# Performance work log

Hardware: AMD Instinct MI355X
Metric: run time of the kernel (lower is better)

## Reference

```python
import jax, jax.numpy as jnp
import numpy as np

N, E, G = 50000, 250000, 512
I_DIM, H, E_DIM = 32, 32, 16


def setup_inputs() -> dict:
    key = jax.random.key(0)
    ks = jax.random.split(key, 16)
    f32 = jnp.float32

    def w(k, shape, fan_in):
        return (jax.random.normal(k, shape, f32) / np.float32(np.sqrt(fan_in)))

    return {
        "x": jax.random.normal(ks[0], (N, I_DIM), f32),
        "edge_attr": jax.random.normal(ks[1], (E, E_DIM), f32),
        "edge_index": jax.random.randint(ks[2], (2, E), 0, N),
        "batch": jnp.sort(jax.random.randint(ks[3], (N,), 0, G)),
        "alpha": jnp.float32(1.0),
        # lin0
        "W0": w(ks[4], (I_DIM, H), I_DIM), "b0": jnp.zeros((H,), f32),
        # NNConv edge-weight MLP: Linear(e,h) -> ReLU -> Linear(h, h*h)
        "We1": w(ks[5], (E_DIM, H), E_DIM), "be1": jnp.zeros((H,), f32),
        "We2": w(ks[6], (H, H * H), H) * 0.1, "be2": jnp.zeros((H * H,), f32),
        # NNConv root weight + bias
        "Wroot": w(ks[7], (H, H), H), "bconv": jnp.zeros((H,), f32),
        # GRU (torch layout: gates [r,z,n] stacked -> 3H rows)
        "Wih": w(ks[8], (3 * H, H), H), "bih": jnp.zeros((3 * H,), f32),
        "Whh": w(ks[9], (3 * H, H), H), "bhh": jnp.zeros((3 * H,), f32),
        # lin1 head (label)
        "W1a": w(ks[10], (H, H), H), "b1a": jnp.zeros((H,), f32),
        "W1b": w(ks[11], (H, 1), H), "b1b": jnp.zeros((1,), f32),
        # lin2 head (domain)
        "W2a": w(ks[12], (H, H), H), "b2a": jnp.zeros((H,), f32),
        "W2b": w(ks[13], (H, 2), H), "b2b": jnp.zeros((2,), f32),
    }


def _segment_mean(vals, ids, num_segments):
    s = jax.ops.segment_sum(vals, ids, num_segments=num_segments)
    cnt = jax.ops.segment_sum(jnp.ones((vals.shape[0], 1), vals.dtype), ids,
                              num_segments=num_segments)
    return s / jnp.maximum(cnt, 1.0)


def reference(x, edge_attr, edge_index, batch, alpha,
              W0, b0, We1, be1, We2, be2, Wroot, bconv,
              Wih, bih, Whh, bhh, W1a, b1a, W1b, b1b, W2a, b2a, W2b, b2b):
    n_nodes = x.shape[0]
    src, dst = edge_index[0], edge_index[1]

    # lin0
    out = jax.nn.relu(x @ W0 + b0)          # [N, H]
    h = out                                   # GRU hidden (single layer, 1 step)

    # edge MLP -> per-edge [H, H] weights (constant across the 3 iterations)
    ew = jax.nn.relu(edge_attr @ We1 + be1) @ We2 + be2   # [E, H*H]
    ew = ew.reshape(-1, H, H)                              # [E, H, H]

    for _ in range(3):
        # NNConv: gather source states, per-edge matmul, scatter-mean to dst
        msg = jnp.einsum('eh,eho->eo', out[src], ew)       # [E, H]
        agg = _segment_mean(msg, dst, n_nodes)             # [N, H]
        m = jax.nn.relu(agg + out @ Wroot + bconv)         # [N, H]
        # GRU step (torch gate order r, z, n)
        gi = m @ Wih.T + bih
        gh = h @ Whh.T + bhh
        r = jax.nn.sigmoid(gi[:, :H] + gh[:, :H])
        z = jax.nn.sigmoid(gi[:, H:2 * H] + gh[:, H:2 * H])
        n = jnp.tanh(gi[:, 2 * H:] + r * gh[:, 2 * H:])
        h = (1.0 - z) * n + z * h
        out = h

    # gradient reversal is identity in forward
    num_graphs = G
    pooled = _segment_mean(out, batch, num_graphs)          # [G, H]

    label_out = (jax.nn.relu(pooled @ W1a + b1a) @ W1b + b1b).reshape(-1)  # [G]
    domain_out = jax.nn.relu(pooled @ W2a + b2a) @ W2b + b2b               # [G, 2]
    return label_out, jax.nn.log_softmax(domain_out, axis=1)
```

## Files before the change

kernel.cpp:

```cpp
#include <hip/hip_runtime.h>

typedef unsigned short u16;
typedef unsigned int u32;

#define NN 50000
#define EE 250000
#define GG 512

typedef __bf16 bf16x8 __attribute__((ext_vector_type(8)));
typedef float  f32x4  __attribute__((ext_vector_type(4)));

__device__ __forceinline__ u16 f2bfu(float f) {
    __bf16 b = (__bf16)f; u16 u; __builtin_memcpy(&u, &b, 2); return u;
}
__device__ __forceinline__ float sigf(float x) { return 1.f / (1.f + expf(-x)); }

__global__ void prep_B(const float* __restrict__ We2, const float* __restrict__ be2,
                       u16* __restrict__ Bg) {
    int idx = blockIdx.x * blockDim.x + threadIdx.x;
    if (idx >= 33 * 1024) return;
    int kk = idx >> 10, off = idx & 1023;
    int ct = off >> 9, l = (off >> 3) & 63, j = off & 7;
    int q = l >> 4, c = l & 15, o = c + 16 * ct;
    float v;
    if (kk < 32) v = We2[(32 * kk + 8 * q + j) * 32 + o];
    else         v = be2[(8 * q + j) * 32 + o];
    Bg[idx] = f2bfu(v);
}

__global__ void prep_WT(const float* __restrict__ Wih, const float* __restrict__ Whh,
                        float4* __restrict__ wta, float2* __restrict__ wtb) {
    int t = blockIdx.x * blockDim.x + threadIdx.x;
    if (t >= 1024) return;
    int k = t >> 5, j = t & 31;
    wta[t] = make_float4(Wih[j * 32 + k], Wih[(32 + j) * 32 + k],
                         Wih[(64 + j) * 32 + k], Whh[j * 32 + k]);
    wtb[t] = make_float2(Whh[(32 + j) * 32 + k], Whh[(64 + j) * 32 + k]);
}

__global__ void prep_edges(const float* __restrict__ ea, const float* __restrict__ We1,
                           const float* __restrict__ be1, u16* __restrict__ tmat) {
    int e = blockIdx.x * blockDim.x + threadIdx.x;
    if (e >= EE) return;
    const float4* ep = (const float4*)(ea + (size_t)e * 16);
    float a[16];
#pragma unroll
    for (int i = 0; i < 4; i++) {
        float4 v = ep[i];
        a[4 * i] = v.x; a[4 * i + 1] = v.y; a[4 * i + 2] = v.z; a[4 * i + 3] = v.w;
    }
    u32 outw[16];
#pragma unroll
    for (int p = 0; p < 16; p++) {
        float acc0 = be1[2 * p], acc1 = be1[2 * p + 1];
#pragma unroll
        for (int k = 0; k < 16; k++) {
            acc0 += a[k] * We1[k * 32 + 2 * p];
            acc1 += a[k] * We1[k * 32 + 2 * p + 1];
        }
        acc0 = fmaxf(acc0, 0.f); acc1 = fmaxf(acc1, 0.f);
        outw[p] = (u32)f2bfu(acc0) | ((u32)f2bfu(acc1) << 16);
    }
    uint4* op = (uint4*)(tmat + (size_t)e * 32);
#pragma unroll
    for (int i = 0; i < 4; i++)
        op[i] = make_uint4(outw[4 * i], outw[4 * i + 1], outw[4 * i + 2], outw[4 * i + 3]);
}

__global__ void lin0_k(const float* __restrict__ x, const float* __restrict__ W0,
                       const float* __restrict__ b0, float* __restrict__ hf,
                       u16* __restrict__ cur) {
    int n = blockIdx.x * blockDim.x + threadIdx.x;
    if (n >= NN) return;
    const float4* xp = (const float4*)(x + (size_t)n * 32);
    float a[32];
#pragma unroll
    for (int i = 0; i < 8; i++) {
        float4 v = xp[i];
        a[4 * i] = v.x; a[4 * i + 1] = v.y; a[4 * i + 2] = v.z; a[4 * i + 3] = v.w;
    }
    float o[32];
#pragma unroll 4
    for (int c = 0; c < 32; c++) {
        float acc = b0[c];
#pragma unroll
        for (int k = 0; k < 32; k++) acc += a[k] * W0[k * 32 + c];
        o[c] = fmaxf(acc, 0.f);
    }
    float4* hp = (float4*)(hf + (size_t)n * 32);
#pragma unroll
    for (int i = 0; i < 8; i++) hp[i] = make_float4(o[4 * i], o[4 * i + 1], o[4 * i + 2], o[4 * i + 3]);
    uint4* cp = (uint4*)(cur + (size_t)n * 32);
#pragma unroll
    for (int i = 0; i < 4; i++) {
        u32 p0 = (u32)f2bfu(o[8 * i + 0]) | ((u32)f2bfu(o[8 * i + 1]) << 16);
        u32 p1 = (u32)f2bfu(o[8 * i + 2]) | ((u32)f2bfu(o[8 * i + 3]) << 16);
        u32 p2 = (u32)f2bfu(o[8 * i + 4]) | ((u32)f2bfu(o[8 * i + 5]) << 16);
        u32 p3 = (u32)f2bfu(o[8 * i + 6]) | ((u32)f2bfu(o[8 * i + 7]) << 16);
        cp[i] = make_uint4(p0, p1, p2, p3);
    }
}

__global__ void hist_k(const int* __restrict__ ei, const int* __restrict__ batch,
                       int* __restrict__ degc, int* __restrict__ gcnt) {
    int i = blockIdx.x * blockDim.x + threadIdx.x;
    if (i < EE) atomicAdd(degc + ei[EE + i], 1);
    if (i < NN) atomicAdd(gcnt + batch[i], 1);
}

__global__ void degfin_k(const int* __restrict__ degc, float* __restrict__ dinv) {
    int n = blockIdx.x * blockDim.x + threadIdx.x;
    if (n >= NN) return;
    int c = degc[n];
    dinv[n] = 1.f / (float)(c > 0 ? c : 1);
}

__global__ __launch_bounds__(512) void msg_k(const u16* __restrict__ cur,
                                             const u16* __restrict__ tmat,
                                             const int* __restrict__ ei,
                                             const u16* __restrict__ Bg,
                                             float* __restrict__ agg) {
    __shared__ uint4 Bl[4096];
    const uint4* Bgv = (const uint4*)Bg;
    for (int i = threadIdx.x; i < 4096; i += 512) Bl[i] = Bgv[i];
    __syncthreads();
    const u16* Bl16 = (const u16*)Bl;

    int l = threadIdx.x & 63;
    int q = l >> 4, r = l & 15;
    int wid = (blockIdx.x * blockDim.x + threadIdx.x) >> 6;
    int nw  = (gridDim.x * blockDim.x) >> 6;

    for (int tile = wid; tile < EE / 16; tile += nw) {
        int eb = tile * 16;
        int srow = ei[eb + r];
        bf16x8 sv = *reinterpret_cast<const bf16x8*>(cur + (size_t)srow * 32 + q * 8);
        float sf[8];
#pragma unroll
        for (int j = 0; j < 8; j++) sf[j] = (float)sv[j];
        const uint4* tp = reinterpret_cast<const uint4*>(tmat + (size_t)(eb + r) * 32);
        f32x4 acc0 = {0.f, 0.f, 0.f, 0.f}, acc1 = {0.f, 0.f, 0.f, 0.f};
#pragma unroll
        for (int kq = 0; kq < 4; kq++) {
            uint4 tw4 = tp[kq];
            u32 tws[4] = {tw4.x, tw4.y, tw4.z, tw4.w};
#pragma unroll
            for (int du = 0; du < 4; du++) {
                u32 w = tws[du];
#pragma unroll
                for (int hl = 0; hl < 2; hl++) {
                    int kk = kq * 8 + du * 2 + hl;
                    float tf = __uint_as_float(hl ? (w & 0xffff0000u) : (w << 16));
                    bf16x8 av;
#pragma unroll
                    for (int j = 0; j < 8; j++) av[j] = (__bf16)(tf * sf[j]);
                    bf16x8 b0 = *reinterpret_cast<const bf16x8*>(Bl16 + kk * 1024 + l * 8);
                    bf16x8 b1 = *reinterpret_cast<const bf16x8*>(Bl16 + kk * 1024 + 512 + l * 8);
                    acc0 = __builtin_amdgcn_mfma_f32_16x16x32_bf16(av, b0, acc0, 0, 0, 0);
                    acc1 = __builtin_amdgcn_mfma_f32_16x16x32_bf16(av, b1, acc1, 0, 0, 0);
                }
            }
        }
        {
            bf16x8 b0 = *reinterpret_cast<const bf16x8*>(Bg + 32 * 1024 + l * 8);
            bf16x8 b1 = *reinterpret_cast<const bf16x8*>(Bg + 32 * 1024 + 512 + l * 8);
            acc0 = __builtin_amdgcn_mfma_f32_16x16x32_bf16(sv, b0, acc0, 0, 0, 0);
            acc1 = __builtin_amdgcn_mfma_f32_16x16x32_bf16(sv, b1, acc1, 0, 0, 0);
        }
#pragma unroll
        for (int j = 0; j < 4; j++) {
            int d = ei[EE + eb + 4 * q + j];
            atomicAdd(agg + (size_t)d * 32 + r,      acc0[j]);
            atomicAdd(agg + (size_t)d * 32 + 16 + r, acc1[j]);
        }
    }
}

__global__ __launch_bounds__(512) void node_update_v4(
        float* __restrict__ hf, u16* __restrict__ cur,
        const float* __restrict__ agg, const float* __restrict__ dinv,
        const float* __restrict__ Wroot, const float* __restrict__ bconv,
        const float4* __restrict__ wta_g, const float2* __restrict__ wtb_g,
        const float* __restrict__ bih, const float* __restrict__ bhh) {
    __shared__ float  wroot_l[1024];
    __shared__ float4 wta_l[1024];
    __shared__ float2 wtb_l[1024];
    __shared__ float  h_l[32 * 66];
    __shared__ float  m_l[32 * 66];
    __shared__ float  bias_l[192];

    const int t = threadIdx.x;
    const int w = t >> 6;
    const int lane = t & 63;
    const int nb = blockIdx.x * 64;
    const int n = nb + lane;
    const int nc = (n < NN) ? n : (NN - 1);

    if (t < 256) ((float4*)wroot_l)[t] = ((const float4*)Wroot)[t];
    wta_l[t] = wta_g[t]; wta_l[t + 512] = wta_g[t + 512];
    ((float4*)wtb_l)[t] = ((const float4*)wtb_g)[t];
    if (t < 192) bias_l[t] = (t < 96) ? bih[t] : bhh[t - 96];

    {
        const int nl = t >> 3, ch = t & 7;
        const int ng = nb + nl;
        const int ngc = (ng < NN) ? ng : (NN - 1);
        float4 v = *(const float4*)(hf + (size_t)ngc * 32 + ch * 4);
        h_l[(ch * 4 + 0) * 66 + nl] = v.x;
        h_l[(ch * 4 + 1) * 66 + nl] = v.y;
        h_l[(ch * 4 + 2) * 66 + nl] = v.z;
        h_l[(ch * 4 + 3) * 66 + nl] = v.w;
    }
    __syncthreads();

    const int c0 = w * 4;
    {
        const float di = dinv[nc];
        float4 ag = *(const float4*)(agg + (size_t)nc * 32 + c0);
        float a0 = bconv[c0 + 0] + ag.x * di;
        float a1 = bconv[c0 + 1] + ag.y * di;
        float a2 = bconv[c0 + 2] + ag.z * di;
        float a3 = bconv[c0 + 3] + ag.w * di;
#pragma unroll 4
        for (int k = 0; k < 32; k++) {
            float hk = h_l[k * 66 + lane];
            float4 wr = *(const float4*)&wroot_l[k * 32 + c0];
            a0 = fmaf(hk, wr.x, a0); a1 = fmaf(hk, wr.y, a1);
            a2 = fmaf(hk, wr.z, a2); a3 = fmaf(hk, wr.w, a3);
        }
        m_l[(c0 + 0) * 66 + lane] = fmaxf(a0, 0.f);
        m_l[(c0 + 1) * 66 + lane] = fmaxf(a1, 0.f);
        m_l[(c0 + 2) * 66 + lane] = fmaxf(a2, 0.f);
        m_l[(c0 + 3) * 66 + lane] = fmaxf(a3, 0.f);
    }
    __syncthreads();

    float outv[4];
#pragma unroll
    for (int half = 0; half < 2; half++) {
        const int j0 = c0 + half * 2;
        float air0 = 0.f, aiz0 = 0.f, ain0 = 0.f, ahr0 = 0.f, ahz0 = 0.f, ahn0 = 0.f;
        float air1 = 0.f, aiz1 = 0.f, ain1 = 0.f, ahr1 = 0.f, ahz1 = 0.f, ahn1 = 0.f;
#pragma unroll 4
        for (int k = 0; k < 32; k++) {
            float mk = m_l[k * 66 + lane];
            float hk = h_l[k * 66 + lane];
            float4 wa0 = wta_l[k * 32 + j0];
            float2 wb0 = wtb_l[k * 32 + j0];
            float4 wa1 = wta_l[k * 32 + j0 + 1];
            float2 wb1 = wtb_l[k * 32 + j0 + 1];
            air0 = fmaf(mk, wa0.x, air0); aiz0 = fmaf(mk, wa0.y, aiz0);
            ain0 = fmaf(mk, wa0.z, ain0); ahr0 = fmaf(hk, wa0.w, ahr0);
            ahz0 = fmaf(hk, wb0.x, ahz0); ahn0 = fmaf(hk, wb0.y, ahn0);
            air1 = fmaf(mk, wa1.x, air1); aiz1 = fmaf(mk, wa1.y, aiz1);
            ain1 = fmaf(mk, wa1.z, ain1); ahr1 = fmaf(hk, wa1.w, ahr1);
            ahz1 = fmaf(hk, wb1.x, ahz1); ahn1 = fmaf(hk, wb1.y, ahn1);
        }
#pragma unroll
        for (int jj = 0; jj < 2; jj++) {
            const int j = j0 + jj;
            float air = jj ? air1 : air0, aiz = jj ? aiz1 : aiz0, ain = jj ? ain1 : ain0;
            float ahr = jj ? ahr1 : ahr0, ahz = jj ? ahz1 : ahz0, ahn = jj ? ahn1 : ahn0;
            float r = sigf(air + ahr + bias_l[j] + bias_l[96 + j]);
            float z = sigf(aiz + ahz + bias_l[32 + j] + bias_l[128 + j]);
            float g = tanhf(ain + bias_l[64 + j] + r * (ahn + bias_l[160 + j]));
            float ho = h_l[j * 66 + lane];
            outv[half * 2 + jj] = (1.f - z) * g + z * ho;
        }
    }
    __syncthreads();

#pragma unroll
    for (int i = 0; i < 4; i++) m_l[(c0 + i) * 66 + lane] = outv[i];
    __syncthreads();

    {
        const int nl = t >> 3, q = (t & 7) * 4;
        const int ng = nb + nl;
        if (ng < NN) {
            float4 v = make_float4(m_l[(q + 0) * 66 + nl], m_l[(q + 1) * 66 + nl],
                                   m_l[(q + 2) * 66 + nl], m_l[(q + 3) * 66 + nl]);
            *(float4*)(hf + (size_t)ng * 32 + q) = v;
            u32 p0 = (u32)f2bfu(v.x) | ((u32)f2bfu(v.y) << 16);
            u32 p1 = (u32)f2bfu(v.z) | ((u32)f2bfu(v.w) << 16);
            *(uint2*)(cur + (size_t)ng * 32 + q) = make_uint2(p0, p1);
        }
    }
}

__global__ void pool_k(const float* __restrict__ hf, const int* __restrict__ batch,
                       float* __restrict__ gsum) {
    int n = blockIdx.x * blockDim.x + threadIdx.x;
    if (n >= NN) return;
    int g = batch[n];
#pragma unroll 8
    for (int o = 0; o < 32; o++) atomicAdd(gsum + g * 32 + o, hf[(size_t)n * 32 + o]);
}

__global__ void head_k(const float* __restrict__ gsum, const int* __restrict__ gcnt,
                       const float* __restrict__ W1a, const float* __restrict__ b1a,
                       const float* __restrict__ W1b, const float* __restrict__ b1b,
                       const float* __restrict__ W2a, const float* __restrict__ b2a,
                       const float* __restrict__ W2b, const float* __restrict__ b2b,
                       float* __restrict__ dout) {
    int g = blockIdx.x * blockDim.x + threadIdx.x;
    if (g >= GG) return;
    int c0 = gcnt[g];
    float rc = 1.f / (float)(c0 > 0 ? c0 : 1);
    float p[32];
#pragma unroll
    for (int i = 0; i < 32; i++) p[i] = gsum[g * 32 + i] * rc;
    float lab = b1b[0];
#pragma unroll 4
    for (int c = 0; c < 32; c++) {
        float acc = b1a[c];
#pragma unroll
        for (int k = 0; k < 32; k++) acc += p[k] * W1a[k * 32 + c];
        lab += fmaxf(acc, 0.f) * W1b[c];
    }
    float d0 = b2b[0], d1 = b2b[1];
#pragma unroll 4
    for (int c = 0; c < 32; c++) {
        float acc = b2a[c];
#pragma unroll
        for (int k = 0; k < 32; k++) acc += p[k] * W2a[k * 32 + c];
        float t = fmaxf(acc, 0.f);
        d0 += t * W2b[c * 2];
        d1 += t * W2b[c * 2 + 1];
    }
    float mx = fmaxf(d0, d1);
    float ls = mx + logf(expf(d0 - mx) + expf(d1 - mx));
    dout[g] = lab;
    dout[GG + g * 2]     = d0 - ls;
    dout[GG + g * 2 + 1] = d1 - ls;
}

extern "C" void kernel_launch(void* const* d_in, const int* in_sizes, int n_in,
                              void* d_out, int out_size, void* d_ws, size_t ws_size,
                              hipStream_t stream) {
    const float* x   = (const float*)d_in[0];
    const float* ea  = (const float*)d_in[1];
    const int* ei    = (const int*)d_in[2];
    const int* batch = (const int*)d_in[3];
    const float* W0 = (const float*)d_in[5],  *b0 = (const float*)d_in[6];
    const float* We1 = (const float*)d_in[7], *be1 = (const float*)d_in[8];
    const float* We2 = (const float*)d_in[9], *be2 = (const float*)d_in[10];
    const float* Wroot = (const float*)d_in[11], *bconv = (const float*)d_in[12];
    const float* Wih = (const float*)d_in[13], *bih = (const float*)d_in[14];
    const float* Whh = (const float*)d_in[15], *bhh = (const float*)d_in[16];
    const float* W1a = (const float*)d_in[17], *b1a = (const float*)d_in[18];
    const float* W1b = (const float*)d_in[19], *b1b = (const float*)d_in[20];
    const float* W2a = (const float*)d_in[21], *b2a = (const float*)d_in[22];
    const float* W2b = (const float*)d_in[23], *b2b = (const float*)d_in[24];
    float* dout = (float*)d_out;

    char* w = (char*)d_ws;
    u16*   tmat = (u16*)w;    w += (size_t)EE * 32 * 2;
    u16*   Bg   = (u16*)w;    w += 33 * 1024 * 2 + 512;
    float* hf   = (float*)w;  w += (size_t)NN * 32 * 4;
    u16*   cur  = (u16*)w;    w += (size_t)NN * 32 * 2;
    float* agg  = (float*)w;  w += (size_t)NN * 32 * 4;
    float* dinv = (float*)w;  w += 200192;
    int*   degc = (int*)w;    w += 200192;
    float* gsum = (float*)w;  w += (size_t)GG * 32 * 4;
    int*   gcnt = (int*)w;    w += 2048;
    float4* wta_g = (float4*)w; w += 1024 * 16;
    float2* wtb_g = (float2*)w; w += 1024 * 8;

    hipMemsetAsync(degc, 0, NN * 4, stream);
    hipMemsetAsync(gcnt, 0, GG * 4, stream);
    hipMemsetAsync(gsum, 0, GG * 32 * 4, stream);

    prep_B<<<132, 256, 0, stream>>>(We2, be2, Bg);
    prep_WT<<<4, 256, 0, stream>>>(Wih, Whh, wta_g, wtb_g);
    prep_edges<<<(EE + 255) / 256, 256, 0, stream>>>(ea, We1, be1, tmat);
    lin0_k<<<(NN + 255) / 256, 256, 0, stream>>>(x, W0, b0, hf, cur);
    hist_k<<<(EE + 255) / 256, 256, 0, stream>>>(ei, batch, degc, gcnt);
    degfin_k<<<(NN + 255) / 256, 256, 0, stream>>>(degc, dinv);

    for (int it = 0; it < 3; it++) {
        hipMemsetAsync(agg, 0, (size_t)NN * 32 * 4, stream);
        msg_k<<<512, 512, 0, stream>>>(cur, tmat, ei, Bg, agg);
        node_update_v4<<<(NN + 63) / 64, 512, 0, stream>>>(hf, cur, agg, dinv,
                                                           Wroot, bconv, wta_g, wtb_g, bih, bhh);
    }

    pool_k<<<(NN + 255) / 256, 256, 0, stream>>>(hf, batch, gsum);
    head_k<<<2, 256, 0, stream>>>(gsum, gcnt, W1a, b1a, W1b, b1b, W2a, b2a, W2b, b2b, dout);
}
```

Before: 713.6 us.

## Sort edges by destination via counting sort; coalesce atomics in msg and pooling

Adds a counting sort of edges by destination (histogram, two-level scan, scatter) and writes the per-edge hidden features and source/destination arrays in that sorted order. The message kernel then reads sorted src/dst and merges consecutive equal-destination contributions in registers before issuing atomics, which cuts atomic traffic and improves locality of the agg writes. Pooling is rewritten so each wavefront walks contiguous nodes and flushes only when the graph id changes, instead of doing one atomic per node per feature. Extra preprocessing kernels and a scatter with atomics add one-off cost, and summation order now differs.

```diff
diff --git a/kernel.cpp b/kernel.cpp
--- a/kernel.cpp
+++ b/kernel.cpp
@@ -38,8 +38,72 @@
     wtb[t] = make_float2(Whh[(32 + j) * 32 + k], Whh[(64 + j) * 32 + k]);
 }
 
+__global__ void hist_k(const int* __restrict__ ei, const int* __restrict__ batch,
+                       int* __restrict__ degc, int* __restrict__ gcnt) {
+    int i = blockIdx.x * blockDim.x + threadIdx.x;
+    if (i < EE) atomicAdd(degc + ei[EE + i], 1);
+    if (i < NN) atomicAdd(gcnt + batch[i], 1);
+}
+
+__global__ __launch_bounds__(512) void scan_blk_k(const int* __restrict__ degc,
+                                                  int* __restrict__ cursor,
+                                                  int* __restrict__ bsum) {
+    __shared__ int s[512];
+    int tid = threadIdx.x, i = blockIdx.x * 512 + tid;
+    int v = (i < NN) ? degc[i] : 0;
+    s[tid] = v; __syncthreads();
+#pragma unroll
+    for (int off = 1; off < 512; off <<= 1) {
+        int t2 = (tid >= off) ? s[tid - off] : 0;
+        __syncthreads();
+        s[tid] += t2;
+        __syncthreads();
+    }
+    if (i < NN) cursor[i] = s[tid] - v;
+    if (tid == 511) bsum[blockIdx.x] = s[511];
+}
+
+__global__ void scan_top_k(const int* __restrict__ bsum, int* __restrict__ boffs) {
+    __shared__ int s[128];
+    int tid = threadIdx.x;
+    int v = (tid < 98) ? bsum[tid] : 0;
+    s[tid] = v; __syncthreads();
+#pragma unroll
+    for (int off = 1; off < 128; off <<= 1) {
+        int t2 = (tid >= off) ? s[tid - off] : 0;
+        __syncthreads();
+        s[tid] += t2;
+        __syncthreads();
+    }
+    if (tid < 98) boffs[tid] = s[tid] - v;
+}
+
+__global__ __launch_bounds__(512) void scan_fix_k(int* __restrict__ cursor,
+                                                  const int* __restrict__ boffs,
+                                                  const int* __restrict__ degc,
+                                                  float* __restrict__ dinv) {
+    int i = blockIdx.x * 512 + threadIdx.x;
+    if (i >= NN) return;
+    cursor[i] += boffs[i >> 9];
+    int c = degc[i];
+    dinv[i] = 1.f / (float)(c > 0 ? c : 1);
+}
+
+__global__ void scatter_k(const int* __restrict__ ei, int* __restrict__ cursor,
+                          int* __restrict__ posOf, int* __restrict__ srcs,
+                          int* __restrict__ dsts) {
+    int e = blockIdx.x * blockDim.x + threadIdx.x;
+    if (e >= EE) return;
+    int d = ei[EE + e];
+    int p = atomicAdd(cursor + d, 1);
+    posOf[e] = p;
+    srcs[p] = ei[e];
+    dsts[p] = d;
+}
+
 __global__ void prep_edges(const float* __restrict__ ea, const float* __restrict__ We1,
-                           const float* __restrict__ be1, u16* __restrict__ tmat) {
+                           const float* __restrict__ be1, const int* __restrict__ posOf,
+                           u16* __restrict__ tmat) {
     int e = blockIdx.x * blockDim.x + threadIdx.x;
     if (e >= EE) return;
     const float4* ep = (const float4*)(ea + (size_t)e * 16);
@@ -61,7 +125,7 @@
         acc0 = fmaxf(acc0, 0.f); acc1 = fmaxf(acc1, 0.f);
         outw[p] = (u32)f2bfu(acc0) | ((u32)f2bfu(acc1) << 16);
     }
-    uint4* op = (uint4*)(tmat + (size_t)e * 32);
+    uint4* op = (uint4*)(tmat + (size_t)posOf[e] * 32);
 #pragma unroll
     for (int i = 0; i < 4; i++)
         op[i] = make_uint4(outw[4 * i], outw[4 * i + 1], outw[4 * i + 2], outw[4 * i + 3]);
@@ -101,23 +165,10 @@
     }
 }
 
-__global__ void hist_k(const int* __restrict__ ei, const int* __restrict__ batch,
-                       int* __restrict__ degc, int* __restrict__ gcnt) {
-    int i = blockIdx.x * blockDim.x + threadIdx.x;
-    if (i < EE) atomicAdd(degc + ei[EE + i], 1);
-    if (i < NN) atomicAdd(gcnt + batch[i], 1);
-}
-
-__global__ void degfin_k(const int* __restrict__ degc, float* __restrict__ dinv) {
-    int n = blockIdx.x * blockDim.x + threadIdx.x;
-    if (n >= NN) return;
-    int c = degc[n];
-    dinv[n] = 1.f / (float)(c > 0 ? c : 1);
-}
-
 __global__ __launch_bounds__(512) void msg_k(const u16* __restrict__ cur,
                                              const u16* __restrict__ tmat,
-                                             const int* __restrict__ ei,
+                                             const int* __restrict__ srcs,
+                                             const int* __restrict__ dsts,
                                              const u16* __restrict__ Bg,
                                              float* __restrict__ agg) {
     __shared__ uint4 Bl[4096];
@@ -133,7 +184,7 @@
 
     for (int tile = wid; tile < EE / 16; tile += nw) {
         int eb = tile * 16;
-        int srow = ei[eb + r];
+        int srow = srcs[eb + r];
         bf16x8 sv = *reinterpret_cast<const bf16x8*>(cur + (size_t)srow * 32 + q * 8);
         float sf[8];
 #pragma unroll
@@ -167,11 +218,30 @@
             acc0 = __builtin_amdgcn_mfma_f32_16x16x32_bf16(sv, b0, acc0, 0, 0, 0);
             acc1 = __builtin_amdgcn_mfma_f32_16x16x32_bf16(sv, b1, acc1, 0, 0, 0);
         }
-#pragma unroll
-        for (int j = 0; j < 4; j++) {
-            int d = ei[EE + eb + 4 * q + j];
-            atomicAdd(agg + (size_t)d * 32 + r,      acc0[j]);
-            atomicAdd(agg + (size_t)d * 32 + 16 + r, acc1[j]);
+        {
+            int d0 = dsts[eb + 4 * q + 0], d1 = dsts[eb + 4 * q + 1];
+            int d2 = dsts[eb + 4 * q + 2], d3 = dsts[eb + 4 * q + 3];
+            float ca = acc0[0], cb = acc1[0];
+            if (d0 != d1) {
+                atomicAdd(agg + (size_t)d0 * 32 + r, ca);
+                atomicAdd(agg + (size_t)d0 * 32 + 16 + r, cb);
+                ca = 0.f; cb = 0.f;
+            }
+            ca += acc0[1]; cb += acc1[1];
+            if (d1 != d2) {
+                atomicAdd(agg + (size_t)d1 * 32 + r, ca);
+                atomicAdd(agg + (size_t)d1 * 32 + 16 + r, cb);
+                ca = 0.f; cb = 0.f;
+            }
+            ca += acc0[2]; cb += acc1[2];
+            if (d2 != d3) {
+                atomicAdd(agg + (size_t)d2 * 32 + r, ca);
+                atomicAdd(agg + (size_t)d2 * 32 + 16 + r, cb);
+                ca = 0.f; cb = 0.f;
+            }
+            ca += acc0[3]; cb += acc1[3];
+            atomicAdd(agg + (size_t)d3 * 32 + r, ca);
+            atomicAdd(agg + (size_t)d3 * 32 + 16 + r, cb);
         }
     }
 }
@@ -288,13 +358,30 @@
     }
 }
 
-__global__ void pool_k(const float* __restrict__ hf, const int* __restrict__ batch,
-                       float* __restrict__ gsum) {
-    int n = blockIdx.x * blockDim.x + threadIdx.x;
-    if (n >= NN) return;
-    int g = batch[n];
-#pragma unroll 8
-    for (int o = 0; o < 32; o++) atomicAdd(gsum + g * 32 + o, hf[(size_t)n * 32 + o]);
+__global__ __launch_bounds__(256) void pool_k2(const float* __restrict__ hf,
+                                               const int* __restrict__ batch,
+                                               float* __restrict__ gsum) {
+    int wv = (blockIdx.x * 256 + threadIdx.x) >> 6;
+    int lane = threadIdx.x & 63;
+    int sub = lane >> 5, o = lane & 31;
+    int base = wv * 256;
+    if (base >= NN) return;
+    float acc = 0.f; int gcur = -1;
+#pragma unroll 4
+    for (int i = 0; i < 128; i++) {
+        int n = base + 2 * i + sub;
+        if (n < NN) {
+            int g = batch[n];
+            float v = hf[(size_t)n * 32 + o];
+            if (g != gcur) {
+                if (gcur >= 0) atomicAdd(gsum + gcur * 32 + o, acc);
+                gcur = g; acc = v;
+            } else {
+                acc += v;
+            }
+        }
+    }
+    if (gcur >= 0) atomicAdd(gsum + gcur * 32 + o, acc);
 }
 
 __global__ void head_k(const float* __restrict__ gsum, const int* __restrict__ gcnt,
@@ -366,25 +453,35 @@
     int*   gcnt = (int*)w;    w += 2048;
     float4* wta_g = (float4*)w; w += 1024 * 16;
     float2* wtb_g = (float2*)w; w += 1024 * 8;
+    int*   cursor = (int*)w;  w += 200192;
+    int*   posOf  = (int*)w;  w += (size_t)EE * 4;
+    int*   srcs   = (int*)w;  w += (size_t)EE * 4;
+    int*   dsts   = (int*)w;  w += (size_t)EE * 4;
+    int*   bsum   = (int*)w;  w += 512;
+    int*   boffs  = (int*)w;  w += 512;
 
     hipMemsetAsync(degc, 0, NN * 4, stream);
     hipMemsetAsync(gcnt, 0, GG * 4, stream);
     hipMemsetAsync(gsum, 0, GG * 32 * 4, stream);
 
+    hist_k<<<(EE + 255) / 256, 256, 0, stream>>>(ei, batch, degc, gcnt);
+    scan_blk_k<<<98, 512, 0, stream>>>(degc, cursor, bsum);
+    scan_top_k<<<1, 128, 0, stream>>>(bsum, boffs);
+    scan_fix_k<<<98, 512, 0, stream>>>(cursor, boffs, degc, dinv);
+    scatter_k<<<(EE + 255) / 256, 256, 0, stream>>>(ei, cursor, posOf, srcs, dsts);
+
     prep_B<<<132, 256, 0, stream>>>(We2, be2, Bg);
     prep_WT<<<4, 256, 0, stream>>>(Wih, Whh, wta_g, wtb_g);
-    prep_edges<<<(EE + 255) / 256, 256, 0, stream>>>(ea, We1, be1, tmat);
+    prep_edges<<<(EE + 255) / 256, 256, 0, stream>>>(ea, We1, be1, posOf, tmat);
     lin0_k<<<(NN + 255) / 256, 256, 0, stream>>>(x, W0, b0, hf, cur);
-    hist_k<<<(EE + 255) / 256, 256, 0, stream>>>(ei, batch, degc, gcnt);
-    degfin_k<<<(NN + 255) / 256, 256, 0, stream>>>(degc, dinv);
 
     for (int it = 0; it < 3; it++) {
         hipMemsetAsync(agg, 0, (size_t)NN * 32 * 4, stream);
-        msg_k<<<512, 512, 0, stream>>>(cur, tmat, ei, Bg, agg);
+        msg_k<<<512, 512, 0, stream>>>(cur, tmat, srcs, dsts, Bg, agg);
         node_update_v4<<<(NN + 63) / 64, 512, 0, stream>>>(hf, cur, agg, dinv,
                                                            Wroot, bconv, wta_g, wtb_g, bih, bhh);
     }
 
-    pool_k<<<(NN + 255) / 256, 256, 0, stream>>>(hf, batch, gsum);
+    pool_k2<<<49, 256, 0, stream>>>(hf, batch, gsum);
     head_k<<<2, 256, 0, stream>>>(gsum, gcnt, W1a, b1a, W1b, b1b, W2a, b2a, W2b, b2b, dout);
 }
```

Measured after the change: 638.8 us. 1.12x faster.
